# Performance work log

Measured on AMD Instinct MI355X. Metric: run time of the kernel, lower is better.

The kernel has to match this reference:

```python
import jax, jax.numpy as jnp
import numpy as np

D_MODEL = 1024
NUM_HEADS = 16
HEAD_DIM = D_MODEL // NUM_HEADS
D_FF = 4096
B, S = 4, 2048
EPS = 1e-5


def layernorm(x, gamma, beta):
    mu = jnp.mean(x, axis=-1, keepdims=True)
    var = jnp.mean(jnp.square(x - mu), axis=-1, keepdims=True)
    return (x - mu) * jax.lax.rsqrt(var + EPS) * gamma + beta


def setup_inputs() -> dict:
    key = jax.random.key(0)
    ks = jax.random.split(key, 16)
    s_in = 1.0 / np.sqrt(D_MODEL)
    s_ff = 1.0 / np.sqrt(D_FF)
    return {
        "x": jax.random.normal(ks[0], (B, S, D_MODEL), jnp.float32),
        "Wq": jax.random.normal(ks[1], (D_MODEL, D_MODEL), jnp.float32) * s_in,
        "bq": jnp.zeros((D_MODEL,), jnp.float32),
        "Wk": jax.random.normal(ks[2], (D_MODEL, D_MODEL), jnp.float32) * s_in,
        "bk": jnp.zeros((D_MODEL,), jnp.float32),
        "Wv": jax.random.normal(ks[3], (D_MODEL, D_MODEL), jnp.float32) * s_in,
        "bv": jnp.zeros((D_MODEL,), jnp.float32),
        "Wo": jax.random.normal(ks[4], (D_MODEL, D_MODEL), jnp.float32) * s_in,
        "bo": jnp.zeros((D_MODEL,), jnp.float32),
        "W1": jax.random.normal(ks[5], (D_MODEL, D_FF), jnp.float32) * s_in,
        "b1": jnp.zeros((D_FF,), jnp.float32),
        "W2": jax.random.normal(ks[6], (D_FF, D_MODEL), jnp.float32) * s_ff,
        "b2": jnp.zeros((D_MODEL,), jnp.float32),
        "g1": jnp.ones((D_MODEL,), jnp.float32),
        "be1": jnp.zeros((D_MODEL,), jnp.float32),
        "g2": jnp.ones((D_MODEL,), jnp.float32),
        "be2": jnp.zeros((D_MODEL,), jnp.float32),
    }


def reference(x, Wq, bq, Wk, bk, Wv, bv, Wo, bo, W1, b1, W2, b2, g1, be1, g2, be2):
    # multi-head self-attention (dropout is identity at eval)
    def split_heads(t):  # [B,S,D] -> [B,H,S,hd]
        return t.reshape(B, S, NUM_HEADS, HEAD_DIM).transpose(0, 2, 1, 3)

    q = split_heads(x @ Wq + bq)
    k = split_heads(x @ Wk + bk)
    v = split_heads(x @ Wv + bv)
    scores = jnp.einsum("bhqd,bhkd->bhqk", q, k) / np.sqrt(HEAD_DIM)
    attn = jax.nn.softmax(scores, axis=-1)
    out = jnp.einsum("bhqk,bhkd->bhqd", attn, v)
    out = out.transpose(0, 2, 1, 3).reshape(B, S, D_MODEL)
    attn_out = out @ Wo + bo

    h = layernorm(x + attn_out, g1, be1)
    ff = jax.nn.relu(h @ W1 + b1) @ W2 + b2
    return layernorm(h + ff, g2, be2)
```

## Files before the change

### kernel.cpp

```cpp
#include <hip/hip_runtime.h>
#include <hip/hip_bf16.h>


#define DM    1024
#define DFF   4096
#define NH    16
#define HD    64
#define BATCH 4
#define SEQ   2048
#define TOK   (BATCH * SEQ)

typedef __attribute__((ext_vector_type(8))) __bf16 bf16x8;
typedef __attribute__((ext_vector_type(4))) float f32x4;
typedef __attribute__((ext_vector_type(16))) float f32x16;
typedef __attribute__((ext_vector_type(4))) unsigned short u16x4;

typedef const __attribute__((address_space(1))) unsigned int* gas1_t;
typedef __attribute__((address_space(3))) unsigned int* las3_t;

__device__ __forceinline__ void gl_lds16(const void* g, void* l) {
  __builtin_amdgcn_global_load_lds((gas1_t)g, (las3_t)l, 16, 0, 0);
}

__device__ __forceinline__ unsigned short f2bu(float x) {
  return __builtin_bit_cast(unsigned short, __float2bfloat16(x));
}

__device__ __forceinline__ unsigned pk_bf16_trunc(float hi, float lo) {
  return __builtin_amdgcn_perm(__builtin_bit_cast(unsigned, hi),
                               __builtin_bit_cast(unsigned, lo), 0x07060302u);
}

__global__ __launch_bounds__(256) void cast_bf16(
    const float* __restrict__ in, unsigned short* __restrict__ out, int n4) {
  int i = blockIdx.x * 256 + threadIdx.x;
  if (i >= n4) return;
  float4 v = ((const float4*)in)[i];
  u16x4 o = {f2bu(v.x), f2bu(v.y), f2bu(v.z), f2bu(v.w)};
  ((u16x4*)out)[i] = o;
}

__global__ __launch_bounds__(256) void transpose_cast(
    const float* __restrict__ in, unsigned short* __restrict__ out, int K, int N) {
  __shared__ float tile[32][33];
  int n0 = blockIdx.x * 32, k0 = blockIdx.y * 32;
  int tx = threadIdx.x, ty = threadIdx.y;
#pragma unroll
  for (int i = 0; i < 4; ++i)
    tile[ty + 8 * i][tx] = in[(size_t)(k0 + ty + 8 * i) * N + n0 + tx];
  __syncthreads();
#pragma unroll
  for (int i = 0; i < 4; ++i)
    out[(size_t)(n0 + ty + 8 * i) * K + k0 + tx] = f2bu(tile[tx][ty + 8 * i]);
}

__global__ __launch_bounds__(256) void transpose_cast4(
    const float* __restrict__ A0, const float* __restrict__ A1,
    const float* __restrict__ A2, const float* __restrict__ A3,
    unsigned short* __restrict__ O0, unsigned short* __restrict__ O1,
    unsigned short* __restrict__ O2, unsigned short* __restrict__ O3) {
  __shared__ float tile[32][33];
  const float* in; unsigned short* out;
  switch (blockIdx.z) {
    case 0: in = A0; out = O0; break;
    case 1: in = A1; out = O1; break;
    case 2: in = A2; out = O2; break;
    default: in = A3; out = O3; break;
  }
  int n0 = blockIdx.x * 32, k0 = blockIdx.y * 32;
  int tx = threadIdx.x, ty = threadIdx.y;
#pragma unroll
  for (int i = 0; i < 4; ++i)
    tile[ty + 8 * i][tx] = in[(size_t)(k0 + ty + 8 * i) * DM + n0 + tx];
  __syncthreads();
#pragma unroll
  for (int i = 0; i < 4; ++i)
    out[(size_t)(n0 + ty + 8 * i) * DM + k0 + tx] = f2bu(tile[tx][ty + 8 * i]);
}

__device__ __forceinline__ void mma8(const bf16x8 a0, const bf16x8 a1,
                                     const bf16x8 b, f32x16* c0, f32x16* c1) {
  *c0 = __builtin_amdgcn_mfma_f32_32x32x16_bf16(a0, b, *c0, 0, 0, 0);
  *c1 = __builtin_amdgcn_mfma_f32_32x32x16_bf16(a1, b, *c1, 0, 0, 0);
}

__device__ __forceinline__ void mainloop256(
    const unsigned short* __restrict__ A, int lda,
    const unsigned short* __restrict__ Bt, int ldb, int Kl,
    int m0, int n0, unsigned short* As, unsigned short* Bs,
    f32x16 acc[2][2][2]) {
  const int tid = threadIdx.x, lane = tid & 63, w = tid >> 6;
  const int l31 = lane & 31, khalf = lane >> 5;
  const int wr = w >> 2, wc = w & 3;
  const int rA0 = wr * 64 + l31, rA1 = rA0 + 32, rB = wc * 32 + l31;

  const unsigned short* pa[2][2];
  const unsigned short* pb[2][2];
#pragma unroll
  for (int h = 0; h < 2; ++h)
#pragma unroll
    for (int i = 0; i < 2; ++i) {
      const int g = (i * 8 + w) * 64 + lane;
      const int r = g >> 3;
      const int cs = ((g & 7) ^ (r & 7)) * 8;
      pa[h][i] = A + (size_t)(m0 + h * 128 + r) * lda + cs;
      pb[h][i] = Bt + (size_t)(n0 + h * 128 + r) * ldb + cs;
    }
  const int wofsB = w * 1024;

  bf16x8 aF[2][4], b0[4], b1[4];

#define STA(BUF, H, I) \
  gl_lds16(pa[H][I], (char*)As + (BUF) * 32768 + (H) * 16384 + (I) * 8192 + wofsB)
#define STB(BUF, H, I) \
  gl_lds16(pb[H][I], (char*)Bs + (BUF) * 32768 + (H) * 16384 + (I) * 8192 + wofsB)
#define ADV_A(H) { pa[H][0] += 64; pa[H][1] += 64; }
#define ADV_B(H) { pb[H][0] += 64; pb[H][1] += 64; }

#define RD_A(BUFB, H)                                                         \
  { const char* Ah = (const char*)As + (BUFB) + (H) * 16384;                  \
    _Pragma("unroll") for (int ks = 0; ks < 4; ++ks) {                        \
      const int c = ks * 2 + khalf;                                           \
      aF[0][ks] = *(const bf16x8*)(Ah + rA0 * 128 + ((c ^ (rA0 & 7)) << 4));  \
      aF[1][ks] = *(const bf16x8*)(Ah + rA1 * 128 + ((c ^ (rA1 & 7)) << 4));  \
    } }
#define RD_B(DST, BUFB, H)                                                    \
  { const char* Bh = (const char*)Bs + (BUFB) + (H) * 16384;                  \
    _Pragma("unroll") for (int ks = 0; ks < 4; ++ks) {                        \
      const int c = ks * 2 + khalf;                                           \
      DST[ks] = *(const bf16x8*)(Bh + rB * 128 + ((c ^ (rB & 7)) << 4));      \
    } }

#define MMA4(QM, QN, BV)                                                      \
  { __builtin_amdgcn_s_setprio(1);                                           \
    _Pragma("unroll") for (int ks = 0; ks < 4; ++ks)                          \
      mma8(aF[0][ks], aF[1][ks], BV[ks], &acc[QM][QN][0], &acc[QM][QN][1]);   \
    __builtin_amdgcn_s_setprio(0); }

#define TILE(BUF, STG, W0, W1, W3)                                            \
  RD_A((BUF) * 32768, 0);                                                     \
  RD_B(b0, (BUF) * 32768, 0);                                                 \
  if (STG) { STA((BUF) ^ 1, 0, 0); STA((BUF) ^ 1, 0, 1); ADV_A(0);            \
             STB((BUF) ^ 1, 0, 0); STB((BUF) ^ 1, 0, 1); ADV_B(0); }          \
  asm volatile(W0 "\n\ts_barrier" ::: "memory");                              \
  MMA4(0, 0, b0);                                                             \
  RD_B(b1, (BUF) * 32768, 1);                                                 \
  if (STG) { STB((BUF) ^ 1, 1, 0); STB((BUF) ^ 1, 1, 1); ADV_B(1); }          \
  asm volatile(W1 "\n\ts_barrier" ::: "memory");                              \
  MMA4(0, 1, b1);                                                             \
  RD_A((BUF) * 32768, 1);                                                     \
  if (STG) { STA((BUF) ^ 1, 1, 0); STA((BUF) ^ 1, 1, 1); ADV_A(1); }          \
  MMA4(1, 1, b1);                                                             \
  RD_B(b0, (BUF) * 32768, 0);                                                 \
  asm volatile(W3 "\n\ts_barrier" ::: "memory");                              \
  MMA4(1, 0, b0);

  STA(0, 0, 0); STA(0, 0, 1); STB(0, 0, 0); STB(0, 0, 1);
  STB(0, 1, 0); STB(0, 1, 1); STA(0, 1, 0); STA(0, 1, 1);
  ADV_A(0); ADV_B(0); ADV_B(1); ADV_A(1);
  asm volatile("s_waitcnt vmcnt(4)\n\ts_barrier" ::: "memory");

  const int NT = Kl >> 6;
  for (int t = 0; t + 2 < NT; t += 2) {
    TILE(0, 1, "s_waitcnt vmcnt(6)", "s_waitcnt vmcnt(6)", "s_waitcnt vmcnt(4)");
    TILE(1, 1, "s_waitcnt vmcnt(6)", "s_waitcnt vmcnt(6)", "s_waitcnt vmcnt(4)");
  }
  TILE(0, 1, "s_waitcnt vmcnt(6)", "s_waitcnt vmcnt(6)", "s_waitcnt vmcnt(4)");
  TILE(1, 0, "s_waitcnt vmcnt(2)", "s_waitcnt vmcnt(0)", "");

#undef TILE
#undef MMA4
#undef RD_B
#undef RD_A
#undef ADV_B
#undef ADV_A
#undef STB
#undef STA
}


__device__ __forceinline__ void xcd_swizzle(int& bx, int& by) {
  const int gx = gridDim.x, nxy = gx * gridDim.y;
  int lin = by * gx + bx;
  lin = (lin & 7) * (nxy >> 3) + (lin >> 3);
  bx = lin % gx;
  by = lin / gx;
}

__global__ __launch_bounds__(512, 2) void gemm256(
    const unsigned short* __restrict__ A, int lda,
    const unsigned short* __restrict__ Bt, int ldb, int Kl,
    const float* __restrict__ bias, void* __restrict__ C0,
    void* __restrict__ C1, int N, float alpha, int relu, int ofp32) {
  __shared__ unsigned short As[32768];
  __shared__ unsigned short Bs[32768];
  const int tid = threadIdx.x, lane = tid & 63, w = tid >> 6;
  const int l31 = lane & 31, khalf = lane >> 5;
  const int wr = w >> 2, wc = w & 3;
  int bx = blockIdx.x, by = blockIdx.y;
  xcd_swizzle(bx, by);
  const int m0 = by * 256, n0 = bx * 256;
  const int koff = blockIdx.z * Kl;
  void* Cout = blockIdx.z ? C1 : C0;
  const float* be = blockIdx.z ? nullptr : bias;

  f32x16 acc[2][2][2];
#pragma unroll
  for (int qm = 0; qm < 2; ++qm)
#pragma unroll
    for (int qn = 0; qn < 2; ++qn)
#pragma unroll
      for (int mi = 0; mi < 2; ++mi)
#pragma unroll
        for (int r = 0; r < 16; ++r) acc[qm][qn][mi][r] = 0.f;

  mainloop256(A + koff, lda, Bt + koff, ldb, Kl, m0, n0, As, Bs, acc);

#pragma unroll
  for (int qn = 0; qn < 2; ++qn) {
    const int col = n0 + qn * 128 + wc * 32 + l31;
    const float bvv = be ? be[col] : 0.f;
#pragma unroll
    for (int qm = 0; qm < 2; ++qm)
#pragma unroll
      for (int mi = 0; mi < 2; ++mi) {
#pragma unroll
        for (int g = 0; g < 4; ++g) {
          const int rbase = m0 + qm * 128 + wr * 64 + mi * 32 + g * 8 + khalf * 4;
#pragma unroll
          for (int r = 0; r < 4; ++r) {
            float val = alpha * (acc[qm][qn][mi][g * 4 + r] + bvv);
            if (relu) val = fmaxf(val, 0.f);
            size_t idx = (size_t)(rbase + r) * N + col;
            if (ofp32) ((float*)Cout)[idx] = val;
            else ((unsigned short*)Cout)[idx] = f2bu(val);
          }
        }
      }
  }
}

#define QSCALE 0.18033688f

__global__ __launch_bounds__(512, 2) void gemm_qkv256(
    const unsigned short* __restrict__ A, const unsigned short* __restrict__ Bt,
    const float* __restrict__ bq, const float* __restrict__ bk,
    const float* __restrict__ bv,
    unsigned short* __restrict__ Qb, unsigned short* __restrict__ Kb,
    unsigned short* __restrict__ Vtg) {
  __shared__ unsigned short As[32768];
  __shared__ unsigned short Bs[32768];
  const int tid = threadIdx.x, lane = tid & 63, w = tid >> 6;
  const int l31 = lane & 31, khalf = lane >> 5;
  const int wr = w >> 2, wc = w & 3;
  int bx = blockIdx.x, by = blockIdx.y;
  xcd_swizzle(bx, by);
  const int m0 = by * 256, n0 = bx * 256;

  f32x16 acc[2][2][2];
#pragma unroll
  for (int qm = 0; qm < 2; ++qm)
#pragma unroll
    for (int qn = 0; qn < 2; ++qn)
#pragma unroll
      for (int mi = 0; mi < 2; ++mi)
#pragma unroll
        for (int r = 0; r < 16; ++r) acc[qm][qn][mi][r] = 0.f;

  mainloop256(A, DM, Bt, DM, DM, m0, n0, As, Bs, acc);

  const int region = n0 >> 10;
  if (region < 2) {
    unsigned short* Out = region ? Kb : Qb;
    const float* bias = region ? bk : bq;
    const float alpha = region ? 1.0f : QSCALE;
#pragma unroll
    for (int qn = 0; qn < 2; ++qn) {
      const int col = (n0 & 1023) + qn * 128 + wc * 32 + l31;
      const float bvv = bias[col];
#pragma unroll
      for (int qm = 0; qm < 2; ++qm)
#pragma unroll
        for (int mi = 0; mi < 2; ++mi) {
#pragma unroll
          for (int g = 0; g < 4; ++g) {
            const int rbase = m0 + qm * 128 + wr * 64 + mi * 32 + g * 8 + khalf * 4;
#pragma unroll
            for (int r = 0; r < 4; ++r)
              Out[(size_t)(rbase + r) * DM + col] =
                  f2bu(alpha * (acc[qm][qn][mi][g * 4 + r] + bvv));
          }
        }
    }
  } else {
#pragma unroll
    for (int qn = 0; qn < 2; ++qn) {
      const int col = (n0 & 1023) + qn * 128 + wc * 32 + l31;
      const float bvv = bv[col];
      const int hh = col >> 6, dl = col & 63;
#pragma unroll
      for (int qm = 0; qm < 2; ++qm)
#pragma unroll
        for (int mi = 0; mi < 2; ++mi) {
#pragma unroll
          for (int g = 0; g < 4; ++g) {
            const int sbase = m0 + qm * 128 + wr * 64 + mi * 32 + g * 8 + khalf * 4;
            const int b_ = sbase >> 11, s0 = sbase & 2047;
            u16x4 pk;
#pragma unroll
            for (int r = 0; r < 4; ++r)
              pk[r] = f2bu(acc[qm][qn][mi][g * 4 + r] + bvv);
            *(u16x4*)(Vtg + ((size_t)((b_ * NH + hh) * HD + dl)) * SEQ + s0) = pk;
          }
        }
    }
  }
}

__global__ __launch_bounds__(256) void attn_kernel(
    const unsigned short* __restrict__ Q, const unsigned short* __restrict__ K,
    const unsigned short* __restrict__ Vtg, unsigned short* __restrict__ O) {
  __shared__ unsigned short Kt[2][64 * 64];
  __shared__ unsigned short Vt[2][64 * 64];
  __shared__ unsigned short Pt[4][32 * 64];
  __shared__ __align__(16) float redL[4][32];

  const int tid = threadIdx.x, lane = tid & 63, w = tid >> 6;
  const int l15 = lane & 15, quad = lane >> 4;
  const int q0 = blockIdx.x * 128;
  const int bh = blockIdx.y, b = bh >> 4, hh = bh & 15;
  const size_t tokbase = (size_t)b * SEQ;

  bf16x8 qf[2][2];
#pragma unroll
  for (int qg = 0; qg < 2; ++qg)
#pragma unroll
    for (int kk = 0; kk < 2; ++kk)
      qf[qg][kk] = *(const bf16x8*)(Q +
          (tokbase + q0 + w * 32 + qg * 16 + l15) * DM + hh * HD + kk * 32 + quad * 8);

  float l_run[2] = {0.f, 0.f};
  f32x4 Oacc[2][4];
#pragma unroll
  for (int qg = 0; qg < 2; ++qg)
#pragma unroll
    for (int nt = 0; nt < 4; ++nt) Oacc[qg][nt] = {0.f, 0.f, 0.f, 0.f};

  char* ptw = (char*)&Pt[w][0];

  int rowS[2], csrcS[2];
#pragma unroll
  for (int i = 0; i < 2; ++i) {
    int f = (i * 4 + w) * 64 + lane;
    rowS[i] = f >> 3;
    csrcS[i] = ((f & 7) ^ (rowS[i] & 7)) * 8;
  }
  const unsigned short* kg[2];
  const unsigned short* vg[2];
  char* ldsK[2][2]; char* ldsV[2][2];
#pragma unroll
  for (int i = 0; i < 2; ++i) {
    kg[i] = K + (tokbase + rowS[i]) * DM + hh * HD + csrcS[i];
    vg[i] = Vtg + ((size_t)bh * HD + rowS[i]) * SEQ + csrcS[i];
#pragma unroll
    for (int bb = 0; bb < 2; ++bb) {
      ldsK[bb][i] = (char*)Kt[bb] + (size_t)((i * 4 + w) * 1024);
      ldsV[bb][i] = (char*)Vt[bb] + (size_t)((i * 4 + w) * 1024);
    }
  }

#pragma unroll
  for (int i = 0; i < 2; ++i) {
    gl_lds16(kg[i], ldsK[0][i]);
    gl_lds16(vg[i], ldsV[0][i]);
    kg[i] += 64 * DM;
    vg[i] += 64;
  }

  for (int j = 0; j < SEQ / 64; ++j) {
    const int buf = j & 1;
    __syncthreads();
    if (j + 1 < SEQ / 64) {
#pragma unroll
      for (int i = 0; i < 2; ++i) {
        gl_lds16(kg[i], ldsK[buf ^ 1][i]);
        gl_lds16(vg[i], ldsV[buf ^ 1][i]);
        kg[i] += 64 * DM;
        vg[i] += 64;
      }
    }

    const char* ktb = (const char*)Kt[buf];
    const char* vtb = (const char*)Vt[buf];

    f32x4 S[2][4];
#pragma unroll
    for (int qg = 0; qg < 2; ++qg)
#pragma unroll
      for (int mt = 0; mt < 4; ++mt) S[qg][mt] = {0.f, 0.f, 0.f, 0.f};
#pragma unroll
    for (int kk = 0; kk < 2; ++kk) {
#pragma unroll
      for (int mt = 0; mt < 4; ++mt) {
        bf16x8 aK = *(const bf16x8*)(ktb + (mt * 16 + l15) * 128 +
                                     (((kk * 4 + quad) ^ (l15 & 7)) * 16));
        S[0][mt] = __builtin_amdgcn_mfma_f32_16x16x32_bf16(aK, qf[0][kk], S[0][mt], 0, 0, 0);
        S[1][mt] = __builtin_amdgcn_mfma_f32_16x16x32_bf16(aK, qf[1][kk], S[1][mt], 0, 0, 0);
      }
    }

#pragma unroll
    for (int qg = 0; qg < 2; ++qg) {
      float rs = 0.f;
#pragma unroll
      for (int mt = 0; mt < 4; ++mt) {
        float p0 = __builtin_amdgcn_exp2f(S[qg][mt][0]);
        float p1 = __builtin_amdgcn_exp2f(S[qg][mt][1]);
        float p2 = __builtin_amdgcn_exp2f(S[qg][mt][2]);
        float p3 = __builtin_amdgcn_exp2f(S[qg][mt][3]);
        rs += (p0 + p1) + (p2 + p3);
        uint2 pk = {pk_bf16_trunc(p1, p0), pk_bf16_trunc(p3, p2)};
        *(uint2*)(ptw + (qg * 16 + l15) * 128 +
                  (((mt * 2 + (quad >> 1)) ^ (l15 & 7)) * 16 + (quad & 1) * 8)) = pk;
      }
      l_run[qg] += rs;
    }

#pragma unroll
    for (int kk = 0; kk < 2; ++kk) {
      bf16x8 aP[2];
#pragma unroll
      for (int qg = 0; qg < 2; ++qg)
        aP[qg] = *(const bf16x8*)(ptw + (qg * 16 + l15) * 128 +
                                  (((kk * 4 + quad) ^ (l15 & 7)) * 16));
#pragma unroll
      for (int nt = 0; nt < 4; ++nt) {
        bf16x8 bV = *(const bf16x8*)(vtb + (nt * 16 + l15) * 128 +
                                     (((kk * 4 + quad) ^ (l15 & 7)) * 16));
        Oacc[0][nt] = __builtin_amdgcn_mfma_f32_16x16x32_bf16(aP[0], bV, Oacc[0][nt], 0, 0, 0);
        Oacc[1][nt] = __builtin_amdgcn_mfma_f32_16x16x32_bf16(aP[1], bV, Oacc[1][nt], 0, 0, 0);
      }
    }
  }

#pragma unroll
  for (int qg = 0; qg < 2; ++qg) {
    l_run[qg] += __shfl_xor(l_run[qg], 16);
    l_run[qg] += __shfl_xor(l_run[qg], 32);
    if (lane < 16) redL[w][qg * 16 + l15] = l_run[qg];
  }
#pragma unroll
  for (int qg = 0; qg < 2; ++qg) {
    f32x4 lv = *(const f32x4*)&redL[w][qg * 16 + quad * 4];
    f32x4 li;
#pragma unroll
    for (int r = 0; r < 4; ++r) li[r] = 1.0f / lv[r];
#pragma unroll
    for (int nt = 0; nt < 4; ++nt)
#pragma unroll
      for (int r = 0; r < 4; ++r) {
        size_t tok = tokbase + q0 + w * 32 + qg * 16 + quad * 4 + r;
        O[tok * DM + hh * HD + nt * 16 + l15] = f2bu(Oacc[qg][nt][r] * li[r]);
      }
  }
}

__global__ __launch_bounds__(256) void ln_res(
    const float* __restrict__ base, const float* __restrict__ d0,
    const float* __restrict__ d1,
    const float* __restrict__ gamma, const float* __restrict__ beta,
    float* __restrict__ outf, unsigned short* __restrict__ outb) {
  __shared__ float red[8];
  const int row = blockIdx.x, tid = threadIdx.x;
  const size_t rb = (size_t)row * DM;
  float4 xv = ((const float4*)(base + rb))[tid];
  float4 dv = ((const float4*)(d0 + rb))[tid];
  float s0 = xv.x + dv.x, s1 = xv.y + dv.y, s2 = xv.z + dv.z, s3 = xv.w + dv.w;
  if (d1) {
    float4 ev = ((const float4*)(d1 + rb))[tid];
    s0 += ev.x; s1 += ev.y; s2 += ev.z; s3 += ev.w;
  }
  float t = s0 + s1 + s2 + s3;
#pragma unroll
  for (int m = 1; m < 64; m <<= 1) t += __shfl_xor(t, m);
  if ((tid & 63) == 0) red[tid >> 6] = t;
  __syncthreads();
  float mu = (red[0] + red[1] + red[2] + red[3]) * (1.0f / DM);
  float dd0 = s0 - mu, dd1 = s1 - mu, dd2 = s2 - mu, dd3 = s3 - mu;
  float v = dd0 * dd0 + dd1 * dd1 + dd2 * dd2 + dd3 * dd3;
#pragma unroll
  for (int m = 1; m < 64; m <<= 1) v += __shfl_xor(v, m);
  if ((tid & 63) == 0) red[4 + (tid >> 6)] = v;
  __syncthreads();
  float var = (red[4] + red[5] + red[6] + red[7]) * (1.0f / DM);
  float rs = rsqrtf(var + 1e-5f);
  float4 gv = ((const float4*)gamma)[tid];
  float4 bv = ((const float4*)beta)[tid];
  float o0 = dd0 * rs * gv.x + bv.x;
  float o1 = dd1 * rs * gv.y + bv.y;
  float o2 = dd2 * rs * gv.z + bv.z;
  float o3 = dd3 * rs * gv.w + bv.w;
  float4 ov = {o0, o1, o2, o3};
  ((float4*)(outf + rb))[tid] = ov;
  if (outb) {
    u16x4 ob = {f2bu(o0), f2bu(o1), f2bu(o2), f2bu(o3)};
    ((u16x4*)(outb + rb))[tid] = ob;
  }
}

extern "C" void kernel_launch(void* const* d_in, const int* in_sizes, int n_in,
                              void* d_out, int out_size, void* d_ws, size_t ws_size,
                              hipStream_t stream) {
  const float* x   = (const float*)d_in[0];
  const float* Wq  = (const float*)d_in[1];  const float* bq  = (const float*)d_in[2];
  const float* Wk  = (const float*)d_in[3];  const float* bk  = (const float*)d_in[4];
  const float* Wv  = (const float*)d_in[5];  const float* bvv = (const float*)d_in[6];
  const float* Wo  = (const float*)d_in[7];  const float* bo  = (const float*)d_in[8];
  const float* W1  = (const float*)d_in[9];  const float* b1  = (const float*)d_in[10];
  const float* W2  = (const float*)d_in[11]; const float* b2  = (const float*)d_in[12];
  const float* g1  = (const float*)d_in[13]; const float* be1 = (const float*)d_in[14];
  const float* g2  = (const float*)d_in[15]; const float* be2 = (const float*)d_in[16];

  char* ws = (char*)d_ws;
  const size_t MB = 1ull << 20;
  unsigned short* xb    = (unsigned short*)(ws + 0 * MB);
  unsigned short* wqkvT = (unsigned short*)(ws + 16 * MB);
  unsigned short* woT   = (unsigned short*)(ws + 22 * MB);
  unsigned short* w1T   = (unsigned short*)(ws + 24 * MB);
  unsigned short* w2T   = (unsigned short*)(ws + 32 * MB);
  unsigned short* Qb    = (unsigned short*)(ws + 40 * MB);
  unsigned short* Kb    = (unsigned short*)(ws + 56 * MB);
  unsigned short* Vtg   = (unsigned short*)(ws + 72 * MB);
  unsigned short* aO    = (unsigned short*)(ws + 104 * MB);
  float*          prj   = (float*)(ws + 120 * MB);
  float*          prj2  = (float*)(ws + 40 * MB);
  float*          h     = (float*)(ws + 152 * MB);
  unsigned short* hb    = (unsigned short*)(ws + 0 * MB);
  unsigned short* ffm   = (unsigned short*)(ws + 40 * MB);
  float*          ffo   = (float*)(ws + 104 * MB);
  float*          ffo2  = (float*)(ws + 0 * MB);
  (void)ws_size; (void)in_sizes; (void)n_in; (void)out_size;

  cast_bf16<<<TOK * DM / 4 / 256, 256, 0, stream>>>(x, xb, TOK * DM / 4);
  transpose_cast4<<<dim3(DM / 32, DM / 32, 4), dim3(32, 8), 0, stream>>>(
      Wq, Wk, Wv, Wo, wqkvT, wqkvT + 1024 * 1024, wqkvT + 2048 * 1024, woT);
  transpose_cast<<<dim3(DFF / 32, DM / 32), dim3(32, 8), 0, stream>>>(W1, w1T, DM, DFF);
  transpose_cast<<<dim3(DM / 32, DFF / 32), dim3(32, 8), 0, stream>>>(W2, w2T, DFF, DM);

  gemm_qkv256<<<dim3(3 * DM / 256, TOK / 256), 512, 0, stream>>>(
      xb, wqkvT, bq, bk, bvv, Qb, Kb, Vtg);

  attn_kernel<<<dim3(SEQ / 128, BATCH * NH), 256, 0, stream>>>(Qb, Kb, Vtg, aO);

  gemm256<<<dim3(DM / 256, TOK / 256, 2), 512, 0, stream>>>(
      aO, DM, woT, DM, DM / 2, bo, prj, prj2, DM, 1.0f, 0, 1);
  ln_res<<<TOK, 256, 0, stream>>>(x, prj, prj2, g1, be1, h, hb);

  gemm256<<<dim3(DFF / 256, TOK / 256, 1), 512, 0, stream>>>(
      hb, DM, w1T, DM, DM, b1, ffm, nullptr, DFF, 1.0f, 1, 0);
  gemm256<<<dim3(DM / 256, TOK / 256, 2), 512, 0, stream>>>(
      ffm, DFF, w2T, DFF, DFF / 2, b2, ffo, ffo2, DM, 1.0f, 0, 1);

  ln_res<<<TOK, 256, 0, stream>>>(h, ffo, ffo2, g2, be2, (float*)d_out, nullptr);
}
```

Measured before the change: 593.9 us.

## Restructure GEMM mainloop into 4-stage K=32 pipeline with 128x64 warp tiles

Rewrites the shared 256x256 GEMM mainloop. The old version double-buffered K=64 tiles in four 128-row quadrants. The new one keeps four K=32 slots in flight, and each warp computes a contiguous 128x64 subtile with 4x2 MFMA accumulators. This deepens prefetch to hide global-load latency and lets each A/B fragment load feed more MFMAs. In exchange there are more barriers per K step, and the epilogue indexing is updated to the new accumulator layout.

```diff
diff --git a/kernel.cpp b/kernel.cpp
--- a/kernel.cpp
+++ b/kernel.cpp
@@ -78,104 +78,99 @@
     out[(size_t)(n0 + ty + 8 * i) * DM + k0 + tx] = f2bu(tile[tx][ty + 8 * i]);
 }
 
-__device__ __forceinline__ void mma8(const bf16x8 a0, const bf16x8 a1,
-                                     const bf16x8 b, f32x16* c0, f32x16* c1) {
-  *c0 = __builtin_amdgcn_mfma_f32_32x32x16_bf16(a0, b, *c0, 0, 0, 0);
-  *c1 = __builtin_amdgcn_mfma_f32_32x32x16_bf16(a1, b, *c1, 0, 0, 0);
-}
-
 __device__ __forceinline__ void mainloop256(
     const unsigned short* __restrict__ A, int lda,
     const unsigned short* __restrict__ Bt, int ldb, int Kl,
     int m0, int n0, unsigned short* As, unsigned short* Bs,
-    f32x16 acc[2][2][2]) {
+    f32x16 acc[4][2]) {
   const int tid = threadIdx.x, lane = tid & 63, w = tid >> 6;
   const int l31 = lane & 31, khalf = lane >> 5;
   const int wr = w >> 2, wc = w & 3;
-  const int rA0 = wr * 64 + l31, rA1 = rA0 + 32, rB = wc * 32 + l31;
-
-  const unsigned short* pa[2][2];
-  const unsigned short* pb[2][2];
-#pragma unroll
-  for (int h = 0; h < 2; ++h)
-#pragma unroll
-    for (int i = 0; i < 2; ++i) {
-      const int g = (i * 8 + w) * 64 + lane;
-      const int r = g >> 3;
-      const int cs = ((g & 7) ^ (r & 7)) * 8;
-      pa[h][i] = A + (size_t)(m0 + h * 128 + r) * lda + cs;
-      pb[h][i] = Bt + (size_t)(n0 + h * 128 + r) * ldb + cs;
-    }
-  const int wofsB = w * 1024;
-
-  bf16x8 aF[2][4], b0[4], b1[4];
-
-#define STA(BUF, H, I) \
-  gl_lds16(pa[H][I], (char*)As + (BUF) * 32768 + (H) * 16384 + (I) * 8192 + wofsB)
-#define STB(BUF, H, I) \
-  gl_lds16(pb[H][I], (char*)Bs + (BUF) * 32768 + (H) * 16384 + (I) * 8192 + wofsB)
-#define ADV_A(H) { pa[H][0] += 64; pa[H][1] += 64; }
-#define ADV_B(H) { pb[H][0] += 64; pb[H][1] += 64; }
-
-#define RD_A(BUFB, H)                                                         \
-  { const char* Ah = (const char*)As + (BUFB) + (H) * 16384;                  \
-    _Pragma("unroll") for (int ks = 0; ks < 4; ++ks) {                        \
-      const int c = ks * 2 + khalf;                                           \
-      aF[0][ks] = *(const bf16x8*)(Ah + rA0 * 128 + ((c ^ (rA0 & 7)) << 4));  \
-      aF[1][ks] = *(const bf16x8*)(Ah + rA1 * 128 + ((c ^ (rA1 & 7)) << 4));  \
+
+  const unsigned short* pa[2];
+  const unsigned short* pb[2];
+#pragma unroll
+  for (int i = 0; i < 2; ++i) {
+    const int row = i * 128 + w * 16 + (lane >> 2);
+    const int cs = ((lane & 3) ^ ((row >> 1) & 3)) * 8;
+    pa[i] = A + (size_t)(m0 + row) * lda + cs;
+    pb[i] = Bt + (size_t)(n0 + row) * ldb + cs;
+  }
+
+  bf16x8 aF[4], bF[2];
+
+#define STAGE_A(SS)                                                           \
+  { gl_lds16(pa[0], (char*)As + (SS) * 16384 + w * 1024);                     \
+    gl_lds16(pa[1], (char*)As + (SS) * 16384 + 8192 + w * 1024);              \
+    pa[0] += 32; pa[1] += 32; }
+#define STAGE_B(SS)                                                           \
+  { gl_lds16(pb[0], (char*)Bs + (SS) * 16384 + w * 1024);                     \
+    gl_lds16(pb[1], (char*)Bs + (SS) * 16384 + 8192 + w * 1024);              \
+    pb[0] += 32; pb[1] += 32; }
+
+#define RD_PH(SLOT, KS)                                                       \
+  { const char* Ab = (const char*)As + (SLOT) * 16384;                        \
+    const char* Bb = (const char*)Bs + (SLOT) * 16384;                        \
+    _Pragma("unroll") for (int rt = 0; rt < 4; ++rt) {                        \
+      const int row = wr * 128 + rt * 32 + l31;                               \
+      aF[rt] = *(const bf16x8*)(Ab + row * 64 +                               \
+                  ((((KS) * 2 + khalf) ^ ((row >> 1) & 3)) << 4));            \
+    }                                                                         \
+    _Pragma("unroll") for (int ni = 0; ni < 2; ++ni) {                        \
+      const int brow = wc * 64 + ni * 32 + l31;                               \
+      bF[ni] = *(const bf16x8*)(Bb + brow * 64 +                              \
+                  ((((KS) * 2 + khalf) ^ ((brow >> 1) & 3)) << 4));           \
     } }
-#define RD_B(DST, BUFB, H)                                                    \
-  { const char* Bh = (const char*)Bs + (BUFB) + (H) * 16384;                  \
-    _Pragma("unroll") for (int ks = 0; ks < 4; ++ks) {                        \
-      const int c = ks * 2 + khalf;                                           \
-      DST[ks] = *(const bf16x8*)(Bh + rB * 128 + ((c ^ (rB & 7)) << 4));      \
-    } }
-
-#define MMA4(QM, QN, BV)                                                      \
-  { __builtin_amdgcn_s_setprio(1);                                           \
-    _Pragma("unroll") for (int ks = 0; ks < 4; ++ks)                          \
-      mma8(aF[0][ks], aF[1][ks], BV[ks], &acc[QM][QN][0], &acc[QM][QN][1]);   \
+
+#define MMA_PH()                                                              \
+  { __builtin_amdgcn_s_setprio(1);                                            \
+    _Pragma("unroll") for (int rt = 0; rt < 4; ++rt)                          \
+      _Pragma("unroll") for (int ni = 0; ni < 2; ++ni)                        \
+        acc[rt][ni] = __builtin_amdgcn_mfma_f32_32x32x16_bf16(                \
+            aF[rt], bF[ni], acc[rt][ni], 0, 0, 0);                            \
     __builtin_amdgcn_s_setprio(0); }
 
-#define TILE(BUF, STG, W0, W1, W3)                                            \
-  RD_A((BUF) * 32768, 0);                                                     \
-  RD_B(b0, (BUF) * 32768, 0);                                                 \
-  if (STG) { STA((BUF) ^ 1, 0, 0); STA((BUF) ^ 1, 0, 1); ADV_A(0);            \
-             STB((BUF) ^ 1, 0, 0); STB((BUF) ^ 1, 0, 1); ADV_B(0); }          \
-  asm volatile(W0 "\n\ts_barrier" ::: "memory");                              \
-  MMA4(0, 0, b0);                                                             \
-  RD_B(b1, (BUF) * 32768, 1);                                                 \
-  if (STG) { STB((BUF) ^ 1, 1, 0); STB((BUF) ^ 1, 1, 1); ADV_B(1); }          \
-  asm volatile(W1 "\n\ts_barrier" ::: "memory");                              \
-  MMA4(0, 1, b1);                                                             \
-  RD_A((BUF) * 32768, 1);                                                     \
-  if (STG) { STA((BUF) ^ 1, 1, 0); STA((BUF) ^ 1, 1, 1); ADV_A(1); }          \
-  MMA4(1, 1, b1);                                                             \
-  RD_B(b0, (BUF) * 32768, 0);                                                 \
-  asm volatile(W3 "\n\ts_barrier" ::: "memory");                              \
-  MMA4(1, 0, b0);
-
-  STA(0, 0, 0); STA(0, 0, 1); STB(0, 0, 0); STB(0, 0, 1);
-  STB(0, 1, 0); STB(0, 1, 1); STA(0, 1, 0); STA(0, 1, 1);
-  ADV_A(0); ADV_B(0); ADV_B(1); ADV_A(1);
-  asm volatile("s_waitcnt vmcnt(4)\n\ts_barrier" ::: "memory");
-
-  const int NT = Kl >> 6;
-  for (int t = 0; t + 2 < NT; t += 2) {
-    TILE(0, 1, "s_waitcnt vmcnt(6)", "s_waitcnt vmcnt(6)", "s_waitcnt vmcnt(4)");
-    TILE(1, 1, "s_waitcnt vmcnt(6)", "s_waitcnt vmcnt(6)", "s_waitcnt vmcnt(4)");
-  }
-  TILE(0, 1, "s_waitcnt vmcnt(6)", "s_waitcnt vmcnt(6)", "s_waitcnt vmcnt(4)");
-  TILE(1, 0, "s_waitcnt vmcnt(2)", "s_waitcnt vmcnt(0)", "");
-
+#define TILE(SLOT, SS, STG, GATESTR)                                          \
+  RD_PH(SLOT, 0);                                                             \
+  if (STG) STAGE_A(SS);                                                       \
+  asm volatile("s_barrier" ::: "memory");                                     \
+  MMA_PH();                                                                   \
+  asm volatile("s_barrier" ::: "memory");                                     \
+  RD_PH(SLOT, 1);                                                             \
+  if (STG) STAGE_B(SS);                                                       \
+  asm volatile("s_barrier" ::: "memory");                                     \
+  MMA_PH();                                                                   \
+  asm volatile(GATESTR ::: "memory");
+
+#define GATE8 "s_waitcnt vmcnt(8)\n\ts_barrier"
+#define GATE4 "s_waitcnt vmcnt(4)\n\ts_barrier"
+#define GATE0 "s_waitcnt vmcnt(0)\n\ts_barrier"
+
+  STAGE_A(0); STAGE_B(0);
+  STAGE_A(1); STAGE_B(1);
+  STAGE_A(2); STAGE_B(2);
+  asm volatile(GATE8 ::: "memory");
+
+  const int NT = Kl >> 5;
+  for (int t = 0; t < NT - 4; t += 4) {
+    TILE(0, 3, 1, GATE8);
+    TILE(1, 0, 1, GATE8);
+    TILE(2, 1, 1, GATE8);
+    TILE(3, 2, 1, GATE8);
+  }
+  TILE(0, 3, 1, GATE8);
+  TILE(1, 0, 0, GATE4);
+  TILE(2, 1, 0, GATE0);
+  TILE(3, 2, 0, "");
+
+#undef GATE0
+#undef GATE4
+#undef GATE8
 #undef TILE
-#undef MMA4
-#undef RD_B
-#undef RD_A
-#undef ADV_B
-#undef ADV_A
-#undef STB
-#undef STA
+#undef MMA_PH
+#undef RD_PH
+#undef STAGE_B
+#undef STAGE_A
 }
 
 
@@ -204,39 +199,35 @@
   void* Cout = blockIdx.z ? C1 : C0;
   const float* be = blockIdx.z ? nullptr : bias;
 
-  f32x16 acc[2][2][2];
-#pragma unroll
-  for (int qm = 0; qm < 2; ++qm)
-#pragma unroll
-    for (int qn = 0; qn < 2; ++qn)
-#pragma unroll
-      for (int mi = 0; mi < 2; ++mi)
-#pragma unroll
-        for (int r = 0; r < 16; ++r) acc[qm][qn][mi][r] = 0.f;
+  f32x16 acc[4][2];
+#pragma unroll
+  for (int rt = 0; rt < 4; ++rt)
+#pragma unroll
+    for (int ni = 0; ni < 2; ++ni)
+#pragma unroll
+      for (int r = 0; r < 16; ++r) acc[rt][ni][r] = 0.f;
 
   mainloop256(A + koff, lda, Bt + koff, ldb, Kl, m0, n0, As, Bs, acc);
 
 #pragma unroll
-  for (int qn = 0; qn < 2; ++qn) {
-    const int col = n0 + qn * 128 + wc * 32 + l31;
+  for (int ni = 0; ni < 2; ++ni) {
+    const int col = n0 + wc * 64 + ni * 32 + l31;
     const float bvv = be ? be[col] : 0.f;
 #pragma unroll
-    for (int qm = 0; qm < 2; ++qm)
-#pragma unroll
-      for (int mi = 0; mi < 2; ++mi) {
-#pragma unroll
-        for (int g = 0; g < 4; ++g) {
-          const int rbase = m0 + qm * 128 + wr * 64 + mi * 32 + g * 8 + khalf * 4;
-#pragma unroll
-          for (int r = 0; r < 4; ++r) {
-            float val = alpha * (acc[qm][qn][mi][g * 4 + r] + bvv);
-            if (relu) val = fmaxf(val, 0.f);
-            size_t idx = (size_t)(rbase + r) * N + col;
-            if (ofp32) ((float*)Cout)[idx] = val;
-            else ((unsigned short*)Cout)[idx] = f2bu(val);
-          }
+    for (int rt = 0; rt < 4; ++rt) {
+#pragma unroll
+      for (int g = 0; g < 4; ++g) {
+        const int rbase = m0 + wr * 128 + rt * 32 + g * 8 + khalf * 4;
+#pragma unroll
+        for (int r = 0; r < 4; ++r) {
+          float val = alpha * (acc[rt][ni][g * 4 + r] + bvv);
+          if (relu) val = fmaxf(val, 0.f);
+          size_t idx = (size_t)(rbase + r) * N + col;
+          if (ofp32) ((float*)Cout)[idx] = val;
+          else ((unsigned short*)Cout)[idx] = f2bu(val);
         }
       }
+    }
   }
 }
 
@@ -257,15 +248,13 @@
   xcd_swizzle(bx, by);
   const int m0 = by * 256, n0 = bx * 256;
 
-  f32x16 acc[2][2][2];
-#pragma unroll
-  for (int qm = 0; qm < 2; ++qm)
-#pragma unroll
-    for (int qn = 0; qn < 2; ++qn)
-#pragma unroll
-      for (int mi = 0; mi < 2; ++mi)
-#pragma unroll
-        for (int r = 0; r < 16; ++r) acc[qm][qn][mi][r] = 0.f;
+  f32x16 acc[4][2];
+#pragma unroll
+  for (int rt = 0; rt < 4; ++rt)
+#pragma unroll
+    for (int ni = 0; ni < 2; ++ni)
+#pragma unroll
+      for (int r = 0; r < 16; ++r) acc[rt][ni][r] = 0.f;
 
   mainloop256(A, DM, Bt, DM, DM, m0, n0, As, Bs, acc);
 
@@ -275,44 +264,40 @@
     const float* bias = region ? bk : bq;
     const float alpha = region ? 1.0f : QSCALE;
 #pragma unroll
-    for (int qn = 0; qn < 2; ++qn) {
-      const int col = (n0 & 1023) + qn * 128 + wc * 32 + l31;
+    for (int ni = 0; ni < 2; ++ni) {
+      const int col = (n0 & 1023) + wc * 64 + ni * 32 + l31;
       const float bvv = bias[col];
 #pragma unroll
-      for (int qm = 0; qm < 2; ++qm)
-#pragma unroll
-        for (int mi = 0; mi < 2; ++mi) {
-#pragma unroll
-          for (int g = 0; g < 4; ++g) {
-            const int rbase = m0 + qm * 128 + wr * 64 + mi * 32 + g * 8 + khalf * 4;
-#pragma unroll
-            for (int r = 0; r < 4; ++r)
-              Out[(size_t)(rbase + r) * DM + col] =
-                  f2bu(alpha * (acc[qm][qn][mi][g * 4 + r] + bvv));
-          }
+      for (int rt = 0; rt < 4; ++rt) {
+#pragma unroll
+        for (int g = 0; g < 4; ++g) {
+          const int rbase = m0 + wr * 128 + rt * 32 + g * 8 + khalf * 4;
+#pragma unroll
+          for (int r = 0; r < 4; ++r)
+            Out[(size_t)(rbase + r) * DM + col] =
+                f2bu(alpha * (acc[rt][ni][g * 4 + r] + bvv));
         }
+      }
     }
   } else {
 #pragma unroll
-    for (int qn = 0; qn < 2; ++qn) {
-      const int col = (n0 & 1023) + qn * 128 + wc * 32 + l31;
+    for (int ni = 0; ni < 2; ++ni) {
+      const int col = (n0 & 1023) + wc * 64 + ni * 32 + l31;
       const float bvv = bv[col];
       const int hh = col >> 6, dl = col & 63;
 #pragma unroll
-      for (int qm = 0; qm < 2; ++qm)
-#pragma unroll
-        for (int mi = 0; mi < 2; ++mi) {
-#pragma unroll
-          for (int g = 0; g < 4; ++g) {
-            const int sbase = m0 + qm * 128 + wr * 64 + mi * 32 + g * 8 + khalf * 4;
-            const int b_ = sbase >> 11, s0 = sbase & 2047;
-            u16x4 pk;
-#pragma unroll
-            for (int r = 0; r < 4; ++r)
-              pk[r] = f2bu(acc[qm][qn][mi][g * 4 + r] + bvv);
-            *(u16x4*)(Vtg + ((size_t)((b_ * NH + hh) * HD + dl)) * SEQ + s0) = pk;
-          }
+      for (int rt = 0; rt < 4; ++rt) {
+#pragma unroll
+        for (int g = 0; g < 4; ++g) {
+          const int sbase = m0 + wr * 128 + rt * 32 + g * 8 + khalf * 4;
+          const int b_ = sbase >> 11, s0 = sbase & 2047;
+          u16x4 pk;
+#pragma unroll
+          for (int r = 0; r < 4; ++r)
+            pk[r] = f2bu(acc[rt][ni][g * 4 + r] + bvv);
+          *(u16x4*)(Vtg + ((size_t)((b_ * NH + hh) * HD + dl)) * SEQ + s0) = pk;
         }
+      }
     }
   }
 }
```

Result: slower. 609.1 us (+2.5%).

## Deepen attention K/V prefetch to four LDS buffers with explicit vmcnt waits

Applied to the files above, without the earlier changes.

The attention kernel's K/V staging goes from a two-slot to a four-slot LDS ring with a prefetch distance of two tiles. Each iteration uses an explicit s_waitcnt vmcnt plus s_barrier so a wave waits only for the tile it is about to consume, which hides more global-load latency. The final softmax row sums are now broadcast with cross-lane shuffles instead of going through an LDS reduction array. This doubles K/V LDS use, which may lower occupancy, and it relies on the hand-counted vmcnt values matching the number of outstanding loads.

```diff
diff --git a/kernel.cpp b/kernel.cpp
--- a/kernel.cpp
+++ b/kernel.cpp
@@ -320,10 +320,9 @@
 __global__ __launch_bounds__(256) void attn_kernel(
     const unsigned short* __restrict__ Q, const unsigned short* __restrict__ K,
     const unsigned short* __restrict__ Vtg, unsigned short* __restrict__ O) {
-  __shared__ unsigned short Kt[2][64 * 64];
-  __shared__ unsigned short Vt[2][64 * 64];
+  __shared__ unsigned short Kt[4][64 * 64];
+  __shared__ unsigned short Vt[4][64 * 64];
   __shared__ unsigned short Pt[4][32 * 64];
-  __shared__ __align__(16) float redL[4][32];
 
   const int tid = threadIdx.x, lane = tid & 63, w = tid >> 6;
   const int l15 = lane & 15, quad = lane >> 4;
@@ -357,41 +356,36 @@
   }
   const unsigned short* kg[2];
   const unsigned short* vg[2];
-  char* ldsK[2][2]; char* ldsV[2][2];
 #pragma unroll
   for (int i = 0; i < 2; ++i) {
     kg[i] = K + (tokbase + rowS[i]) * DM + hh * HD + csrcS[i];
     vg[i] = Vtg + ((size_t)bh * HD + rowS[i]) * SEQ + csrcS[i];
-#pragma unroll
-    for (int bb = 0; bb < 2; ++bb) {
-      ldsK[bb][i] = (char*)Kt[bb] + (size_t)((i * 4 + w) * 1024);
-      ldsV[bb][i] = (char*)Vt[bb] + (size_t)((i * 4 + w) * 1024);
-    }
-  }
-
-#pragma unroll
-  for (int i = 0; i < 2; ++i) {
-    gl_lds16(kg[i], ldsK[0][i]);
-    gl_lds16(vg[i], ldsV[0][i]);
-    kg[i] += 64 * DM;
-    vg[i] += 64;
-  }
-
-  for (int j = 0; j < SEQ / 64; ++j) {
-    const int buf = j & 1;
-    __syncthreads();
-    if (j + 1 < SEQ / 64) {
-#pragma unroll
-      for (int i = 0; i < 2; ++i) {
-        gl_lds16(kg[i], ldsK[buf ^ 1][i]);
-        gl_lds16(vg[i], ldsV[buf ^ 1][i]);
-        kg[i] += 64 * DM;
-        vg[i] += 64;
-      }
-    }
-
-    const char* ktb = (const char*)Kt[buf];
-    const char* vtb = (const char*)Vt[buf];
+  }
+
+#define STAGE_KV(BUF)                                                         \
+  { _Pragma("unroll") for (int i = 0; i < 2; ++i) {                           \
+      gl_lds16(kg[i], (char*)Kt + (BUF) * 8192 + (i * 4 + w) * 1024);         \
+      gl_lds16(vg[i], (char*)Vt + (BUF) * 8192 + (i * 4 + w) * 1024);         \
+      kg[i] += 64 * DM;                                                       \
+      vg[i] += 64;                                                            \
+    } }
+
+  const int NT = SEQ / 64;
+  STAGE_KV(0);
+  STAGE_KV(1);
+
+  for (int j = 0; j < NT; ++j) {
+    const int buf = j & 3;
+    if (j + 2 < NT) STAGE_KV((j + 2) & 3);
+    if (j < NT - 2)
+      asm volatile("s_waitcnt vmcnt(8)\n\ts_barrier" ::: "memory");
+    else if (j == NT - 2)
+      asm volatile("s_waitcnt vmcnt(4)\n\ts_barrier" ::: "memory");
+    else
+      asm volatile("s_waitcnt vmcnt(0)\n\ts_barrier" ::: "memory");
+
+    const char* ktb = (const char*)Kt + buf * 8192;
+    const char* vtb = (const char*)Vt + buf * 8192;
 
     f32x4 S[2][4];
 #pragma unroll
@@ -442,19 +436,18 @@
       }
     }
   }
+#undef STAGE_KV
 
 #pragma unroll
   for (int qg = 0; qg < 2; ++qg) {
     l_run[qg] += __shfl_xor(l_run[qg], 16);
     l_run[qg] += __shfl_xor(l_run[qg], 32);
-    if (lane < 16) redL[w][qg * 16 + l15] = l_run[qg];
   }
 #pragma unroll
   for (int qg = 0; qg < 2; ++qg) {
-    f32x4 lv = *(const f32x4*)&redL[w][qg * 16 + quad * 4];
     f32x4 li;
 #pragma unroll
-    for (int r = 0; r < 4; ++r) li[r] = 1.0f / lv[r];
+    for (int r = 0; r < 4; ++r) li[r] = 1.0f / __shfl(l_run[qg], quad * 4 + r);
 #pragma unroll
     for (int nt = 0; nt < 4; ++nt)
 #pragma unroll
```

New measurement: 590.8 us. Within noise of the previous version (-0.5%).
